# Kernel tuning notes

Hardware: AMD Instinct MI355X
Metric: run time of the kernel (lower is better)

## Reference

```python
import jax, jax.numpy as jnp
import numpy as np

# ---- maxflat pyramid filters (pfilters('maxflat')) ----
def _maxflat_filters():
    sqrt2 = np.sqrt(2.0)
    M1 = M2 = 1.0 / sqrt2
    k1 = 1.0 - sqrt2
    k2 = k3 = M1
    h_half = np.array([0.25 * k2 * k3, 0.5 * k2, 1.0 + 0.5 * k2 * k3]) * M1
    h = np.concatenate([h_half, h_half[:-1][::-1]]) * sqrt2          # len 5
    g_half = np.array([-0.125 * k1 * k2 * k3,
                       0.25 * k1 * k2,
                       -0.5 * k1 - 0.5 * k3 - 0.375 * k1 * k2 * k3,
                       1.0 + 0.5 * k1 * k2]) * M2
    g = np.concatenate([g_half, g_half[:-1][::-1]]) * sqrt2          # len 7
    return h.astype(np.float32), g.astype(np.float32)

# highpass from g, as in wfb2dec: h1 = -g * (-1)**(arange(1,L+1)-c)
def _wfb_filters():
    h, g = _maxflat_filters()
    len_h1 = len(g)                      # 7 (odd)
    c = int(np.floor((len_h1 + 1.0) / 2.0))   # 4
    h1 = (-g * (-1.0) ** (np.arange(1, len_h1 + 1) - c)).astype(np.float32)
    ext_h0 = int(np.floor(len(h) / 2.0))      # 2
    ext_h1 = len_h1 - c + 1                   # 4
    return h, h1, ext_h0, ext_h1

# periodic row filtering along last axis (torch rowfiltering: periodic pad +
# cross-correlation, which F.conv2d / lax conv both compute without flip)
def rowfilt(x, f, ext1):
    L = f.shape[0]
    ext2 = L - ext1 - 1
    W = x.shape[-1]
    xe = jnp.concatenate([x[..., -ext1:], x, x[..., :ext2]], axis=-1)
    y = f[0] * xe[..., 0:W]
    for k in range(1, L):                 # tiny fixed tap loop, fuses fine
        y = y + f[k] * xe[..., k:k + W]
    return y

def colfilt(x, f, ext1):
    return jnp.swapaxes(rowfilt(jnp.swapaxes(x, -1, -2), f, ext1), -1, -2)


def setup_inputs() -> dict:
    key = jax.random.key(0)
    x = jax.random.normal(key, (8, 3, 1024, 1024), dtype=jnp.float32)
    return {"x": x}


def reference(x):
    # Pycontourlet.batch_multi_channel_pdfbdec with pfilt='maxflat',
    # nlevs=[0] -> wfb2dec path: one level of separable wavelet FB with
    # periodic extension; returns [xLL, [xLH, xHL, xHH]] (stacked here).
    h_np, h1_np, e0, e1 = _wfb_filters()
    h = jnp.asarray(h_np)
    h1 = jnp.asarray(h1_np)

    x_L = rowfilt(x, h, e0)[..., ::2]          # [B,C,H,W/2]
    x_H = rowfilt(x, h1, e1)[..., ::2]

    x_LL = colfilt(x_L, h, e0)[..., ::2, :]    # [B,C,H/2,W/2]
    x_LH = colfilt(x_L, h1, e1)[..., ::2, :]
    x_HL = colfilt(x_H, h, e0)[..., ::2, :]
    x_HH = colfilt(x_H, h1, e1)[..., ::2, :]

    return jnp.stack([x_LL, x_LH, x_HL, x_HH])  # [4,B,C,H/2,W/2]
```

## Files before the change

kernel.cpp:

```cpp
#include <hip/hip_runtime.h>


constexpr int H = 1024, W = 1024;
constexpr int NIMG = 24;
constexpr int HOUT = 512, WOUT = 512;
constexpr int BROWS = 16;
constexpr int BCOLS = 64;

__global__ __launch_bounds__(256)
void wfb_kernel(const float* __restrict__ x, float* __restrict__ out) {
    const float h0c[5] = {0.125f, 0.35355339059327373f, 1.25f,
                          0.35355339059327373f, 0.125f};
    const float h1c[7] = {0.025888347648318447f,  0.07322330470336313f,
                          -0.06878156646177083f, -0.8535533905932737f,
                          -0.06878156646177083f,  0.07322330470336313f,
                          0.025888347648318447f};

    const int tid = threadIdx.x;
    const int img = blockIdx.z;
    const int R  = blockIdx.y * BROWS + (tid >> 4);
    const int J0 = blockIdx.x * BCOLS + (tid & 15) * 4;
    const float* __restrict__ xin = x + (size_t)img * H * W;

    const int rb = 2 * R - 4;
    const int cb = 2 * J0 - 4;

    int gc0 = (cb     ) & (W - 1);
    int gc1 = (cb +  4) & (W - 1);
    int gc2 = (cb +  8) & (W - 1);
    int gc3 = (cb + 12) & (W - 1);

    float vA[13], vB[13];
    #pragma unroll
    for (int c = 0; c < 13; ++c) { vA[c] = 0.f; vB[c] = 0.f; }

    float v[16];

    #pragma unroll
    for (int d = 0; d < 7; ++d) {
        const int gr = (rb + d) & (H - 1);
        const float* __restrict__ rowp = xin + ((size_t)gr << 10);
        {
            float4 f0 = *(const float4*)(rowp + gc0);
            float4 f1 = *(const float4*)(rowp + gc1);
            float4 f2 = *(const float4*)(rowp + gc2);
            float4 f3 = *(const float4*)(rowp + gc3);
            v[ 0]=f0.x; v[ 1]=f0.y; v[ 2]=f0.z; v[ 3]=f0.w;
            v[ 4]=f1.x; v[ 5]=f1.y; v[ 6]=f1.z; v[ 7]=f1.w;
            v[ 8]=f2.x; v[ 9]=f2.y; v[10]=f2.z; v[11]=f2.w;
            v[12]=f3.x;
        }
        #pragma unroll
        for (int c = 0; c < 13; ++c) {
            vB[c] += h1c[d] * v[c];
        }
        if (d >= 2) {
            #pragma unroll
            for (int c = 0; c < 13; ++c) {
                vA[c] += h0c[d - 2] * v[c];
            }
        }
    }

    float LL[4], LH[4], HL[4], HH[4];
    #pragma unroll
    for (int u = 0; u < 4; ++u) {
        const float* a = vA + 2 * u;
        const float* b = vB + 2 * u;
        LL[u] = h0c[0]*a[2] + h0c[1]*a[3] + h0c[2]*a[4]
              + h0c[3]*a[5] + h0c[4]*a[6];
        HL[u] = h1c[0]*a[0] + h1c[1]*a[1] + h1c[2]*a[2] + h1c[3]*a[3]
              + h1c[4]*a[4] + h1c[5]*a[5] + h1c[6]*a[6];
        LH[u] = h0c[0]*b[2] + h0c[1]*b[3] + h0c[2]*b[4]
              + h0c[3]*b[5] + h0c[4]*b[6];
        HH[u] = h1c[0]*b[0] + h1c[1]*b[1] + h1c[2]*b[2] + h1c[3]*b[3]
              + h1c[4]*b[4] + h1c[5]*b[5] + h1c[6]*b[6];
    }

    constexpr size_t SB = (size_t)NIMG * HOUT * WOUT;
    float* __restrict__ o = out + (size_t)img * HOUT * WOUT;
    const size_t off = (size_t)R * WOUT + J0;
    *(float4*)(o + 0*SB + off) = make_float4(LL[0], LL[1], LL[2], LL[3]);
    *(float4*)(o + 1*SB + off) = make_float4(LH[0], LH[1], LH[2], LH[3]);
    *(float4*)(o + 2*SB + off) = make_float4(HL[0], HL[1], HL[2], HL[3]);
    *(float4*)(o + 3*SB + off) = make_float4(HH[0], HH[1], HH[2], HH[3]);
}

extern "C" void kernel_launch(void* const* d_in, const int* in_sizes, int n_in,
                              void* d_out, int out_size, void* d_ws, size_t ws_size,
                              hipStream_t stream) {
    const float* x = (const float*)d_in[0];
    float* out = (float*)d_out;
    dim3 grid(WOUT / BCOLS, HOUT / BROWS, NIMG);
    wfb_kernel<<<grid, dim3(256), 0, stream>>>(x, out);
}
```

Before: 187.7 us.

## Stage input tile in LDS via direct global-to-LDS loads

Each block now loads its 37x144 input halo tile into shared memory with global_load_lds 16-byte transfers, then each thread reads its 7x13 window from LDS instead of issuing overlapping global float4 loads. This removes redundant global/L2 traffic from neighbouring threads reading overlapping rows and columns. It adds a block-wide barrier and about 21 KB of LDS per block, which may limit occupancy and serializes the load and compute phases.

```diff
diff --git a/kernel.cpp b/kernel.cpp
--- a/kernel.cpp
+++ b/kernel.cpp
@@ -6,9 +6,16 @@
 constexpr int HOUT = 512, WOUT = 512;
 constexpr int BROWS = 16;
 constexpr int BCOLS = 64;
+constexpr int TROWS = 37;
+constexpr int TSEGS = 36;
+constexpr int NSEG  = TROWS * TSEGS;
+constexpr int NCHUNK = (NSEG + 63) / 64;
+constexpr int ROWF  = TSEGS * 4;
 
 __global__ __launch_bounds__(256)
 void wfb_kernel(const float* __restrict__ x, float* __restrict__ out) {
+    __shared__ __align__(16) float smem[NCHUNK * 256];
+
     const float h0c[5] = {0.125f, 0.35355339059327373f, 1.25f,
                           0.35355339059327373f, 0.125f};
     const float h1c[7] = {0.025888347648318447f,  0.07322330470336313f,
@@ -16,49 +23,52 @@
                           -0.06878156646177083f,  0.07322330470336313f,
                           0.025888347648318447f};
 
-    const int tid = threadIdx.x;
-    const int img = blockIdx.z;
-    const int R  = blockIdx.y * BROWS + (tid >> 4);
-    const int J0 = blockIdx.x * BCOLS + (tid & 15) * 4;
+    const int tid  = threadIdx.x;
+    const int wave = tid >> 6;
+    const int lane = tid & 63;
+    const int img  = blockIdx.z;
+    const int R0   = blockIdx.y * BROWS;
+    const int J0b  = blockIdx.x * BCOLS;
     const float* __restrict__ xin = x + (size_t)img * H * W;
+    const int rb0 = 2 * R0 - 4;
+    const int cb0 = 2 * J0b - 4;
 
-    const int rb = 2 * R - 4;
-    const int cb = 2 * J0 - 4;
+    for (int c = wave; c < NCHUNK; c += 4) {
+        int t  = c * 64 + lane;
+        int r  = t / TSEGS;
+        int s  = t - r * TSEGS;
+        int gr = (rb0 + r) & (H - 1);
+        int gc = (cb0 + 4 * s) & (W - 1);
+        const float* gp = xin + ((size_t)gr << 10) + gc;
+        __builtin_amdgcn_global_load_lds(
+            (const __attribute__((address_space(1))) void*)gp,
+            (__attribute__((address_space(3))) void*)(smem + c * 256),
+            16, 0, 0);
+    }
+    __syncthreads();
 
-    int gc0 = (cb     ) & (W - 1);
-    int gc1 = (cb +  4) & (W - 1);
-    int gc2 = (cb +  8) & (W - 1);
-    int gc3 = (cb + 12) & (W - 1);
+    const int Rl   = tid >> 4;
+    const int colf = (tid & 15) * 8;
 
     float vA[13], vB[13];
     #pragma unroll
     for (int c = 0; c < 13; ++c) { vA[c] = 0.f; vB[c] = 0.f; }
 
-    float v[16];
-
     #pragma unroll
     for (int d = 0; d < 7; ++d) {
-        const int gr = (rb + d) & (H - 1);
-        const float* __restrict__ rowp = xin + ((size_t)gr << 10);
-        {
-            float4 f0 = *(const float4*)(rowp + gc0);
-            float4 f1 = *(const float4*)(rowp + gc1);
-            float4 f2 = *(const float4*)(rowp + gc2);
-            float4 f3 = *(const float4*)(rowp + gc3);
-            v[ 0]=f0.x; v[ 1]=f0.y; v[ 2]=f0.z; v[ 3]=f0.w;
-            v[ 4]=f1.x; v[ 5]=f1.y; v[ 6]=f1.z; v[ 7]=f1.w;
-            v[ 8]=f2.x; v[ 9]=f2.y; v[10]=f2.z; v[11]=f2.w;
-            v[12]=f3.x;
-        }
+        const float* rowp = smem + (2 * Rl + d) * ROWF + colf;
+        float4 f0 = *(const float4*)(rowp);
+        float4 f1 = *(const float4*)(rowp + 4);
+        float4 f2 = *(const float4*)(rowp + 8);
+        float v12 = rowp[12];
+        float v[13] = {f0.x, f0.y, f0.z, f0.w,
+                       f1.x, f1.y, f1.z, f1.w,
+                       f2.x, f2.y, f2.z, f2.w, v12};
         #pragma unroll
-        for (int c = 0; c < 13; ++c) {
-            vB[c] += h1c[d] * v[c];
-        }
+        for (int c = 0; c < 13; ++c) vB[c] += h1c[d] * v[c];
         if (d >= 2) {
             #pragma unroll
-            for (int c = 0; c < 13; ++c) {
-                vA[c] += h0c[d - 2] * v[c];
-            }
+            for (int c = 0; c < 13; ++c) vA[c] += h0c[d - 2] * v[c];
         }
     }
 
@@ -79,6 +89,8 @@
 
     constexpr size_t SB = (size_t)NIMG * HOUT * WOUT;
     float* __restrict__ o = out + (size_t)img * HOUT * WOUT;
+    const int R  = R0 + Rl;
+    const int J0 = J0b + (tid & 15) * 4;
     const size_t off = (size_t)R * WOUT + J0;
     *(float4*)(o + 0*SB + off) = make_float4(LL[0], LL[1], LL[2], LL[3]);
     *(float4*)(o + 1*SB + off) = make_float4(LH[0], LH[1], LH[2], LH[3]);
```

Measured after the change: 175.8 us. -6.3%, faster.
